# Performance work log

Hardware: AMD Instinct MI355X
Metric: run time of the kernel (lower is better)

Reference implementation:

```python
import jax, jax.numpy as jnp
import numpy as np
from jax import lax
import math

POOL = 7
SPATIAL_SCALE = 0.125
SCORE_THRESH = 0.05
NMS_THRESH = 0.5
DET_PER_IMG = 100
NUM_CLASSES = 81
NUM_STAGES = 3
FEAT_CH = 256
CLIP_VAL = math.log(1000.0 / 16)
STDS = ((0.1, 0.1, 0.2, 0.2), (0.05, 0.05, 0.1, 0.1), (0.033, 0.033, 0.067, 0.067))


def setup_inputs() -> dict:
    key = jax.random.key(0)
    ks = jax.random.split(key, 12)
    B, N, img = 2, 512, 512
    features = jax.random.normal(ks[0], (B, FEAT_CH, 64, 64), jnp.float32)
    cx = jax.random.uniform(ks[1], (B, N)) * img
    cy = jax.random.uniform(ks[2], (B, N)) * img
    w = 16.0 + jax.random.uniform(ks[3], (B, N)) * 240.0
    h = 16.0 + jax.random.uniform(ks[4], (B, N)) * 240.0
    proposals = jnp.stack([
        jnp.clip(cx - 0.5 * w, 0.0, img), jnp.clip(cy - 0.5 * h, 0.0, img),
        jnp.clip(cx + 0.5 * w, 0.0, img), jnp.clip(cy + 0.5 * h, 0.0, img)], axis=-1)
    in_dim = FEAT_CH * POOL * POOL
    sc = 0.02
    return {
        'features': features,
        'proposals': proposals,
        'fc1_w': jax.random.normal(ks[5], (NUM_STAGES, in_dim, 1024), jnp.float32) * sc,
        'fc1_b': jnp.zeros((NUM_STAGES, 1024), jnp.float32),
        'fc2_w': jax.random.normal(ks[6], (NUM_STAGES, 1024, 1024), jnp.float32) * sc,
        'fc2_b': jnp.zeros((NUM_STAGES, 1024), jnp.float32),
        'cls_w': jax.random.normal(ks[7], (NUM_STAGES, 1024, NUM_CLASSES), jnp.float32) * sc,
        'cls_b': jnp.zeros((NUM_STAGES, NUM_CLASSES), jnp.float32),
        'bbox_w': jax.random.normal(ks[8], (NUM_STAGES, 1024, 4), jnp.float32) * sc,
        'bbox_b': jnp.zeros((NUM_STAGES, 4), jnp.float32),
        'image_size': 512,
    }


def _bilinear(feat, gx, gy):
    # feat [C,H,W]; gx,gy [N,P,P] float coords
    C, H, W = feat.shape
    x = jnp.clip(gx, 0.0, W - 1.0)
    y = jnp.clip(gy, 0.0, H - 1.0)
    x0f, y0f = jnp.floor(x), jnp.floor(y)
    x0 = x0f.astype(jnp.int32)
    y0 = y0f.astype(jnp.int32)
    x1 = jnp.minimum(x0 + 1, W - 1)
    y1 = jnp.minimum(y0 + 1, H - 1)
    dx = (x - x0f)[None]
    dy = (y - y0f)[None]
    v = (feat[:, y0, x0] * (1 - dy) * (1 - dx) + feat[:, y0, x1] * (1 - dy) * dx
         + feat[:, y1, x0] * dy * (1 - dx) + feat[:, y1, x1] * dy * dx)
    return v  # [C,N,P,P]


def roi_align(feat, boxes):
    # feat [C,H,W], boxes [N,4] in feature-map coords
    x1, y1, x2, y2 = boxes[:, 0], boxes[:, 1], boxes[:, 2], boxes[:, 3]
    bw = jnp.maximum(x2 - x1, 1.0) / POOL
    bh = jnp.maximum(y2 - y1, 1.0) / POOL
    c = jnp.arange(POOL, dtype=boxes.dtype) + 0.5
    xs = x1[:, None] + c * bw[:, None]  # [N,P]
    ys = y1[:, None] + c * bh[:, None]
    N = boxes.shape[0]
    gx = jnp.broadcast_to(xs[:, None, :], (N, POOL, POOL))
    gy = jnp.broadcast_to(ys[:, :, None], (N, POOL, POOL))
    return jnp.transpose(_bilinear(feat, gx, gy), (1, 0, 2, 3))  # [N,C,P,P]


def decode_boxes(proposals, deltas, stds):
    px1, py1, px2, py2 = proposals[:, 0], proposals[:, 1], proposals[:, 2], proposals[:, 3]
    pw = jnp.maximum(px2 - px1, 1e-6)
    ph = jnp.maximum(py2 - py1, 1e-6)
    pcx = px1 + 0.5 * pw
    pcy = py1 + 0.5 * ph
    wx, wy, ww, wh = stds
    dx = deltas[:, 0] * wx
    dy = deltas[:, 1] * wy
    dw = jnp.minimum(deltas[:, 2] * ww, CLIP_VAL)
    dh = jnp.minimum(deltas[:, 3] * wh, CLIP_VAL)
    cx = dx * pw + pcx
    cy = dy * ph + pcy
    w = jnp.exp(dw) * pw
    h = jnp.exp(dh) * ph
    return jnp.stack([cx - 0.5 * w, cy - 0.5 * h, cx + 0.5 * w, cy + 0.5 * h], axis=1)


def clip_boxes(b, img):
    return jnp.stack([jnp.clip(b[:, 0], 0.0, img), jnp.clip(b[:, 1], 0.0, img),
                      jnp.clip(b[:, 2], 0.0, img), jnp.clip(b[:, 3], 0.0, img)], axis=1)


def nms_per_image(boxes, probs, img):
    # boxes [N,4], probs [N,C]
    N, C = probs.shape
    Cm = C - 1  # skip background class 0
    labels = jnp.broadcast_to(jnp.arange(1, C, dtype=jnp.int32), (N, Cm)).reshape(-1)
    b = jnp.broadcast_to(boxes[:, None, :], (N, Cm, 4)).reshape(-1, 4)
    s = probs[:, 1:].reshape(-1)
    ws = b[:, 2] - b[:, 0]
    hs = b[:, 3] - b[:, 1]
    valid = (s > SCORE_THRESH) & (ws >= 1.0) & (hs >= 1.0)
    s = jnp.where(valid, s, -1.0)
    # class-offset trick == batched_nms
    ob = b + (labels.astype(b.dtype) * (img + 2.0))[:, None]
    area = jnp.maximum(ob[:, 2] - ob[:, 0], 0.0) * jnp.maximum(ob[:, 3] - ob[:, 1], 0.0)

    def step(s_live, _):
        i = jnp.argmax(s_live)
        si = s_live[i]
        bi = ob[i]
        ix1 = jnp.maximum(bi[0], ob[:, 0])
        iy1 = jnp.maximum(bi[1], ob[:, 1])
        ix2 = jnp.minimum(bi[2], ob[:, 2])
        iy2 = jnp.minimum(bi[3], ob[:, 3])
        inter = jnp.maximum(ix2 - ix1, 0.0) * jnp.maximum(iy2 - iy1, 0.0)
        iou = inter / (area[i] + area - inter + 1e-9)
        s_live = jnp.where(iou > NMS_THRESH, -1.0, s_live)
        s_live = s_live.at[i].set(-1.0)
        return s_live, (i, si)

    _, (idx, sel_s) = lax.scan(step, s, None, length=DET_PER_IMG)
    flag = sel_s > 0.0
    out_boxes = jnp.where(flag[:, None], b[idx], 0.0)
    out_scores = jnp.where(flag, sel_s, 0.0)
    out_labels = jnp.where(flag, labels[idx], 0)
    return out_boxes, out_scores, out_labels


def reference(features, proposals, fc1_w, fc1_b, fc2_w, fc2_b, cls_w, cls_b, bbox_w, bbox_b, image_size):
    B, Cf, H, W = features.shape
    N = proposals.shape[1]
    img = float(image_size)
    cur = proposals  # [B,N,4]
    logits = None
    for st in range(NUM_STAGES):
        pooled = jax.vmap(lambda f, bx: roi_align(f, bx * SPATIAL_SCALE))(features, cur)  # [B,N,C,P,P]
        x = pooled.reshape(B * N, -1)
        x = jax.nn.relu(x @ fc1_w[st] + fc1_b[st])
        x = jax.nn.relu(x @ fc2_w[st] + fc2_b[st])
        logits = x @ cls_w[st] + cls_b[st]  # [B*N, C]
        deltas = x @ bbox_w[st] + bbox_b[st]  # [B*N, 4]
        dec = clip_boxes(decode_boxes(cur.reshape(-1, 4), deltas, STDS[st]), img)
        cur = dec.reshape(B, N, 4)
    probs = jax.nn.softmax(logits.reshape(B, N, -1), axis=-1)
    boxes, scores, labels = jax.vmap(lambda bb, pp: nms_per_image(bb, pp, img))(cur, probs)
    return boxes, scores, labels
```

## Files before the change

kernel.cpp:

```cpp
#include <hip/hip_runtime.h>
#include <math.h>

#define NPROP 512
#define NB 2
#define NROWS (NB*NPROP)
#define FCH 256
#define FH 64
#define FW 64
#define INDIM (FCH*7*7)
#define HID 1024
#define NCLS 81
#define CAND_PER_IMG (NPROP*(NCLS-1))
#define CLIPV 4.1351666f

typedef _Float16 f16x8 __attribute__((ext_vector_type(8)));
typedef float f32x4 __attribute__((ext_vector_type(4)));
typedef unsigned int u32;
typedef unsigned long long u64;

__device__ __forceinline__ void gload16(const void* g, void* l) {
    __builtin_amdgcn_global_load_lds((const __attribute__((address_space(1))) u32*)g,
                                     (__attribute__((address_space(3))) u32*)l, 16, 0, 0);
}

#define XHI_OFF    0ull
#define XLO_OFF    25690112ull
#define WT1HI_OFF  51380224ull
#define WT1LO_OFF  77070336ull
#define WT2HI_OFF  102760448ull
#define WT2LO_OFF  104857600ull
#define H1HI_OFF   106954752ull
#define H1LO_OFF   109051904ull
#define H2_OFF     111149056ull
#define CWT_OFF    115343360ull
#define BWT_OFF    116338688ull
#define PROBS_OFF  116387840ull
#define CUR_OFF    116719616ull
#define CNT_OFF    116736000ull
#define CCS_OFF    116737024ull
#define CCOB_OFF   117064704ull
#define CCAR_OFF   118375424ull
#define CCBX_OFF   118703104ull
#define CCIX_OFF   120013824ull
#define SVS_OFF    120341504ull
#define SVB_OFF    120423424ull
#define SVI_OFF    120751104ull
#define SVC_OFF    120833024ull
#define PART_OFF   121489408ull

__global__ void init_kernel(int* ccnt) {
    if (threadIdx.x < 160) ccnt[threadIdx.x] = 0;
}

__global__ __launch_bounds__(256) void roi_align_kernel(
    const float* __restrict__ feat, const float* __restrict__ boxes,
    _Float16* __restrict__ Xhi, _Float16* __restrict__ Xlo)
{
    int r = blockIdx.x;
    int b = r >> 9;
    const float* f = feat + (size_t)b * (FCH*FH*FW);
    __shared__ float sb[4];
    __shared__ int   sx0[49], sx1[49], sy0[49], sy1[49];
    __shared__ float sw00[49], sw01[49], sw10[49], sw11[49];
    int tid = threadIdx.x;
    if (tid == 0) {
        float x1 = boxes[r*4+0]*0.125f, y1 = boxes[r*4+1]*0.125f;
        float x2 = boxes[r*4+2]*0.125f, y2 = boxes[r*4+3]*0.125f;
        sb[0] = x1; sb[1] = y1;
        sb[2] = fmaxf(x2-x1, 1.0f) / 7.0f;
        sb[3] = fmaxf(y2-y1, 1.0f) / 7.0f;
    }
    __syncthreads();
    if (tid < 49) {
        int py = tid / 7, px = tid - py*7;
        float gx = sb[0] + ((float)px + 0.5f)*sb[2];
        float gy = sb[1] + ((float)py + 0.5f)*sb[3];
        gx = fminf(fmaxf(gx, 0.0f), 63.0f);
        gy = fminf(fmaxf(gy, 0.0f), 63.0f);
        float x0f = floorf(gx), y0f = floorf(gy);
        int x0 = (int)x0f, y0 = (int)y0f;
        sx0[tid] = x0; sy0[tid] = y0;
        sx1[tid] = min(x0+1, 63); sy1[tid] = min(y0+1, 63);
        float dx = gx - x0f, dy = gy - y0f;
        sw00[tid] = (1.0f-dy)*(1.0f-dx);
        sw01[tid] = (1.0f-dy)*dx;
        sw10[tid] = dy*(1.0f-dx);
        sw11[tid] = dy*dx;
    }
    __syncthreads();
    size_t xbase = (size_t)r * INDIM;
    for (int i = tid; i < INDIM; i += 256) {
        int c = i / 49;
        int p = i - c*49;
        const float* fc = f + c*(FH*FW);
        int r0 = sy0[p]*FW, r1 = sy1[p]*FW;
        float v = fc[r0 + sx0[p]]*sw00[p] + fc[r0 + sx1[p]]*sw01[p]
                + fc[r1 + sx0[p]]*sw10[p] + fc[r1 + sx1[p]]*sw11[p];
        float vs = v * 32.0f;
        _Float16 h = (_Float16)vs;
        Xhi[xbase + i] = h;
        Xlo[xbase + i] = (_Float16)(vs - (float)h);
    }
}

__global__ __launch_bounds__(256) void trans_limb(
    const float* __restrict__ in, _Float16* __restrict__ hi, _Float16* __restrict__ lo,
    int K, int N, float scale)
{
    __shared__ float t[32][33];
    int tx = threadIdx.x & 31, ty = threadIdx.x >> 5;
    int n0 = blockIdx.x << 5, k0 = blockIdx.y << 5;
#pragma unroll
    for (int r = 0; r < 4; ++r)
        t[ty + 8*r][tx] = in[(size_t)(k0 + ty + 8*r)*N + n0 + tx];
    __syncthreads();
#pragma unroll
    for (int r = 0; r < 4; ++r) {
        int n = n0 + ty + 8*r, k = k0 + tx;
        float v = t[tx][ty + 8*r] * scale;
        _Float16 h = (_Float16)v;
        hi[(size_t)n*K + k] = h;
        lo[(size_t)n*K + k] = (_Float16)(v - (float)h);
    }
}

__global__ __launch_bounds__(256) void trans_naive(
    const float* __restrict__ in, float* __restrict__ out, int K, int N, int batch)
{
    int idx = blockIdx.x*256 + threadIdx.x;
    int per = K*N;
    if (idx >= per*batch) return;
    int b = idx / per;
    int rem = idx - b*per;
    int n = rem / K, k = rem - n*K;
    out[idx] = in[(size_t)b*per + (size_t)k*N + n];
}

__global__ __launch_bounds__(256) void mfma_gemm_limb(
    const _Float16* __restrict__ Ahi, const _Float16* __restrict__ Alo,
    const _Float16* __restrict__ Bhi, const _Float16* __restrict__ Blo,
    float* __restrict__ part, int K, int base, int extra, int lognz)
{
    __shared__ __align__(16) _Float16 lds[2][4][512][8];
    const int tid = threadIdx.x;
    const int lane = tid & 63;
    const int w = tid >> 6, wm = w >> 1, wn = w & 1;
    const int kg = lane >> 4, lr = lane & 15;
    const int bid = blockIdx.x;
    const int nzm = (1 << lognz) - 1;
    const int z = bid & nzm;
    const int bx = (bid >> lognz) & 7;
    const int by = bid >> (lognz + 3);
    const int row0 = by << 7, col0 = bx << 7;
    const int zsteps = base + (z < extra ? 1 : 0);
    const int kb0 = (z*base + (z < extra ? z : extra)) * 32;
    const int r_ = tid & 127;
    const int ks1 = tid >> 7;
    const int wb = tid & 192;

    const _Float16* srcA0 = Ahi + (size_t)(row0 + r_) * K + kb0 + ks1*8;
    const _Float16* srcA1 = Alo + (size_t)(row0 + r_) * K + kb0 + ks1*8;
    const _Float16* srcB0 = Bhi + (size_t)(col0 + r_) * K + kb0 + ks1*8;
    const _Float16* srcB1 = Blo + (size_t)(col0 + r_) * K + kb0 + ks1*8;

    f32x4 acc[4][4];
#pragma unroll
    for (int i = 0; i < 4; ++i)
#pragma unroll
        for (int j = 0; j < 4; ++j) acc[i][j] = (f32x4){0.f, 0.f, 0.f, 0.f};

#define STAGE(bf, off) do { \
    _Float16* Lb = &lds[bf][0][0][0]; \
    gload16(srcA0 + (off),      (void*)(Lb + (0*512 +       wb)*8)); \
    gload16(srcA0 + (off) + 16, (void*)(Lb + (0*512 + 256 + wb)*8)); \
    gload16(srcA1 + (off),      (void*)(Lb + (1*512 +       wb)*8)); \
    gload16(srcA1 + (off) + 16, (void*)(Lb + (1*512 + 256 + wb)*8)); \
    gload16(srcB0 + (off),      (void*)(Lb + (2*512 +       wb)*8)); \
    gload16(srcB0 + (off) + 16, (void*)(Lb + (2*512 + 256 + wb)*8)); \
    gload16(srcB1 + (off),      (void*)(Lb + (3*512 +       wb)*8)); \
    gload16(srcB1 + (off) + 16, (void*)(Lb + (3*512 + 256 + wb)*8)); \
} while (0)

    STAGE(0, 0);
    if (1 < zsteps) STAGE(1, 32);
    for (int t = 0; t < zsteps; ++t) {
        if (t + 1 < zsteps) asm volatile("s_waitcnt vmcnt(8)" ::: "memory");
        else                asm volatile("s_waitcnt vmcnt(0)" ::: "memory");
        __builtin_amdgcn_s_barrier();
        const _Float16* Lr = &lds[t & 1][0][0][0];
        f16x8 Ah[4], Al[4], Bh[4], Bl[4];
#pragma unroll
        for (int mi = 0; mi < 4; ++mi) {
            int s = kg*128 + wm*64 + mi*16 + lr;
            Ah[mi] = *(const f16x8*)(Lr + (0*512 + s)*8);
            Al[mi] = *(const f16x8*)(Lr + (1*512 + s)*8);
        }
#pragma unroll
        for (int ni = 0; ni < 4; ++ni) {
            int s = kg*128 + wn*64 + ni*16 + lr;
            Bh[ni] = *(const f16x8*)(Lr + (2*512 + s)*8);
            Bl[ni] = *(const f16x8*)(Lr + (3*512 + s)*8);
        }
        asm volatile("s_waitcnt lgkmcnt(0)" ::: "memory");
        __builtin_amdgcn_sched_barrier(0);
        __builtin_amdgcn_s_barrier();
        if (t + 2 < zsteps) STAGE(t & 1, (t+2)*32);
#pragma unroll
        for (int mi = 0; mi < 4; ++mi)
#pragma unroll
            for (int ni = 0; ni < 4; ++ni) {
                acc[mi][ni] = __builtin_amdgcn_mfma_f32_16x16x32_f16(Ah[mi], Bh[ni], acc[mi][ni], 0, 0, 0);
                acc[mi][ni] = __builtin_amdgcn_mfma_f32_16x16x32_f16(Ah[mi], Bl[ni], acc[mi][ni], 0, 0, 0);
                acc[mi][ni] = __builtin_amdgcn_mfma_f32_16x16x32_f16(Al[mi], Bh[ni], acc[mi][ni], 0, 0, 0);
            }
    }
#undef STAGE

    float* cb = part + ((size_t)z << 20)
              + (size_t)row0*HID + col0 + wn*64 + lr;
#pragma unroll
    for (int mi = 0; mi < 4; ++mi) {
#pragma unroll
        for (int j = 0; j < 4; ++j) {
            int row = wm*64 + mi*16 + kg*4 + j;
            float* pr = cb + (size_t)row*HID;
            pr[0]  = acc[mi][0][j];
            pr[16] = acc[mi][1][j];
            pr[32] = acc[mi][2][j];
            pr[48] = acc[mi][3][j];
        }
    }
}

__global__ __launch_bounds__(256) void reduce_bias_relu(
    const float* __restrict__ part, const float* __restrict__ bias,
    float* __restrict__ out32, _Float16* __restrict__ outhi, _Float16* __restrict__ outlo,
    int nsplit, int mode)
{
    int gid = blockIdx.x*256 + threadIdx.x;
    float s = 0.f;
    for (int p = 0; p < nsplit; ++p) s += part[((size_t)p << 20) + gid];
    s = s * (1.0f/2048.0f) + bias[gid & (HID-1)];
    s = fmaxf(s, 0.f);
    if (mode == 0) {
        out32[gid] = s;
    } else {
        float vs = s * 32.0f;
        _Float16 h = (_Float16)vs;
        outhi[gid] = h;
        outlo[gid] = (_Float16)(vs - (float)h);
    }
}

__global__ __launch_bounds__(512) void heads_kernel(
    const float* __restrict__ X, const float* __restrict__ cwT, const float* __restrict__ cb,
    const float* __restrict__ bwT, const float* __restrict__ bbb,
    float* __restrict__ cur, float* __restrict__ probs,
    const int* __restrict__ img_sz, int stage, int write_probs)
{
    __shared__ float xs[4][1024];
    __shared__ float lg[4][96];
    int tid = threadIdx.x;
    int lr = tid >> 7;
    int j  = tid & 127;
    int row0 = blockIdx.x * 4;
    for (int i = tid; i < 4096; i += 512)
        xs[i >> 10][i & 1023] = X[(size_t)(row0 + (i >> 10))*1024 + (i & 1023)];
    __syncthreads();
    int row = row0 + lr;
    if (j < 85) {
        const float* wrow = (j < 81) ? (cwT + (size_t)j*HID) : (bwT + (size_t)(j-81)*HID);
        float acc = (j < 81) ? cb[j] : bbb[j-81];
        const float4* w4 = (const float4*)wrow;
#pragma unroll 4
        for (int k4 = 0; k4 < 256; ++k4) {
            float4 wv = w4[k4];
            const float* xr = &xs[lr][k4*4];
            acc = fmaf(xr[0], wv.x, acc);
            acc = fmaf(xr[1], wv.y, acc);
            acc = fmaf(xr[2], wv.z, acc);
            acc = fmaf(xr[3], wv.w, acc);
        }
        lg[lr][j] = acc;
    }
    __syncthreads();
    if (j == 0) {
        float img = (float)(*img_sz);
        float px1 = cur[row*4+0], py1 = cur[row*4+1];
        float px2 = cur[row*4+2], py2 = cur[row*4+3];
        float pw = fmaxf(px2-px1, 1e-6f), ph = fmaxf(py2-py1, 1e-6f);
        float pcx = px1 + 0.5f*pw, pcy = py1 + 0.5f*ph;
        float wx, wy, ww, wh;
        if (stage == 0)      { wx=0.1f;   wy=0.1f;   ww=0.2f;   wh=0.2f;   }
        else if (stage == 1) { wx=0.05f;  wy=0.05f;  ww=0.1f;   wh=0.1f;   }
        else                 { wx=0.033f; wy=0.033f; ww=0.067f; wh=0.067f; }
        float dx = lg[lr][81]*wx, dy = lg[lr][82]*wy;
        float dw = fminf(lg[lr][83]*ww, CLIPV);
        float dh = fminf(lg[lr][84]*wh, CLIPV);
        float cx = dx*pw + pcx, cy = dy*ph + pcy;
        float w = expf(dw)*pw, h = expf(dh)*ph;
        cur[row*4+0] = fminf(fmaxf(cx - 0.5f*w, 0.f), img);
        cur[row*4+1] = fminf(fmaxf(cy - 0.5f*h, 0.f), img);
        cur[row*4+2] = fminf(fmaxf(cx + 0.5f*w, 0.f), img);
        cur[row*4+3] = fminf(fmaxf(cy + 0.5f*h, 0.f), img);
    }
    if (write_probs) {
        if (j == 1) {
            float m = lg[lr][0];
            for (int c2 = 1; c2 < 81; ++c2) m = fmaxf(m, lg[lr][c2]);
            float s = 0.f;
            for (int c2 = 0; c2 < 81; ++c2) s += expf(lg[lr][c2] - m);
            lg[lr][88] = m; lg[lr][89] = s;
        }
        __syncthreads();
        if (j < 81)
            probs[(size_t)row*81 + j] = expf(lg[lr][j] - lg[lr][88]) / lg[lr][89];
    }
}

__global__ __launch_bounds__(256) void compact_class(
    const float* __restrict__ probs, const float* __restrict__ cur,
    const int* __restrict__ img_sz, int* __restrict__ ccnt,
    float* __restrict__ ccs, float4* __restrict__ ccob, float* __restrict__ ccar,
    float4* __restrict__ ccbx, int* __restrict__ ccix)
{
    int gid = blockIdx.x*256 + threadIdx.x;
    if (gid >= NB*CAND_PER_IMG) return;
    int b = gid / CAND_PER_IMG;
    int rem = gid - b*CAND_PER_IMG;
    int n = rem / 80;
    int cm = rem - n*80;
    int label = cm + 1;
    int r = b*NPROP + n;
    float s = probs[(size_t)r*81 + label];
    float b0 = cur[r*4+0], b1 = cur[r*4+1], b2 = cur[r*4+2], b3 = cur[r*4+3];
    if (s > 0.05f && (b2 - b0) >= 1.0f && (b3 - b1) >= 1.0f) {
        int cls = b*80 + cm;
        int pos = atomicAdd(&ccnt[cls], 1);
        int base = cls*512 + pos;
        float img = (float)(*img_sz);
        float t = (float)label * (img + 2.0f);
        float o0 = b0+t, o1 = b1+t, o2 = b2+t, o3 = b3+t;
        ccs[base] = s;
        ccob[base] = make_float4(o0, o1, o2, o3);
        ccar[base] = fmaxf(o2-o0, 0.f) * fmaxf(o3-o1, 0.f);
        ccbx[base] = make_float4(b0, b1, b2, b3);
        ccix[base] = rem;
    }
}

__global__ __launch_bounds__(64) void class_nms(
    const int* __restrict__ ccnt, const float* __restrict__ ccs,
    const float4* __restrict__ ccob, const float* __restrict__ ccar,
    const float4* __restrict__ ccbx, const int* __restrict__ ccix,
    float* __restrict__ svs, float4* __restrict__ svb, int* __restrict__ svi,
    int* __restrict__ svc)
{
    int cls = blockIdx.x;
    int Nc = ccnt[cls];
    int base = cls*512;
    int lane = threadIdx.x;
    __shared__ float sel[5];
    float s[8]; float4 ob[8]; float a[8]; int ix[8];
    int cntl = 0;
    for (int j = lane; j < Nc; j += 64) {
        s[cntl] = ccs[base+j]; ob[cntl] = ccob[base+j];
        a[cntl] = ccar[base+j]; ix[cntl] = ccix[base+j];
        ++cntl;
    }
    int svn = 0;
    int rounds = (Nc < 100) ? Nc : 100;
    for (int it = 0; it < rounds; ++it) {
        float bs = -1.f; int bi = 0x7fffffff;
        for (int q = 0; q < cntl; ++q)
            if (s[q] > bs || (s[q] == bs && ix[q] < bi)) { bs = s[q]; bi = ix[q]; }
        for (int off = 32; off > 0; off >>= 1) {
            float os = __shfl_xor(bs, off);
            int oi = __shfl_xor(bi, off);
            if (os > bs || (os == bs && oi < bi)) { bs = os; bi = oi; }
        }
        if (bs <= 0.f) break;
        for (int q = 0; q < cntl; ++q) {
            if (s[q] == bs && ix[q] == bi) {
                sel[0] = ob[q].x; sel[1] = ob[q].y; sel[2] = ob[q].z; sel[3] = ob[q].w;
                sel[4] = a[q];
                int slot = cls*128 + svn;
                svs[slot] = bs;
                svb[slot] = ccbx[base + lane + q*64];
                svi[slot] = bi;
                s[q] = -1.f;
            }
        }
        __syncthreads();
        float bi0 = sel[0], bi1 = sel[1], bi2 = sel[2], bi3 = sel[3], ai = sel[4];
        for (int q = 0; q < cntl; ++q) {
            if (s[q] > 0.f) {
                float ix1 = fmaxf(bi0, ob[q].x), iy1 = fmaxf(bi1, ob[q].y);
                float ix2 = fminf(bi2, ob[q].z), iy2 = fminf(bi3, ob[q].w);
                float inter = fmaxf(ix2-ix1, 0.f) * fmaxf(iy2-iy1, 0.f);
                float iou = inter / (ai + a[q] - inter + 1e-9f);
                if (iou > 0.5f) s[q] = -1.f;
            }
        }
        ++svn;
        __syncthreads();
    }
    if (lane == 0) svc[cls] = svn;
}

__global__ __launch_bounds__(256) void merge_topk(
    const float* __restrict__ svs, const float4* __restrict__ svb,
    const int* __restrict__ svi, const int* __restrict__ svc,
    float* __restrict__ out)
{
    extern __shared__ char smem[];
    u64* keys = (u64*)smem;
    u32* pay  = (u32*)(smem + 65536);
    __shared__ int off[81];
    __shared__ int n2s;
    int b = blockIdx.x, tid = threadIdx.x;
    if (tid == 0) {
        int run = 0;
        for (int c = 0; c < 80; ++c) { off[c] = run; run += svc[b*80 + c]; }
        off[80] = run;
        int n2 = 256;
        while (n2 < run) n2 <<= 1;
        n2s = n2;
    }
    __syncthreads();
    int Ns = off[80], n2 = n2s;
    for (int c = 0; c < 80; ++c) {
        int n = off[c+1] - off[c];
        int srcb = (b*80 + c)*128;
        for (int k = tid; k < n; k += 256) {
            int src = srcb + k;
            keys[off[c] + k] = ((u64)__float_as_uint(svs[src]) << 32)
                             | (u64)(0xFFFFFFFFu - (u32)svi[src]);
            pay[off[c] + k] = src;
        }
    }
    for (int i = Ns + tid; i < n2; i += 256) { keys[i] = 0; pay[i] = 0; }
    __syncthreads();
    for (int k = 2; k <= n2; k <<= 1) {
        for (int j = k >> 1; j > 0; j >>= 1) {
            for (int i = tid; i < n2; i += 256) {
                int l = i ^ j;
                if (l > i) {
                    u64 a = keys[i], bb = keys[l];
                    bool dir = ((i & k) == 0);
                    if ((a < bb) == dir) {
                        keys[i] = bb; keys[l] = a;
                        u32 p = pay[i]; pay[i] = pay[l]; pay[l] = p;
                    }
                }
            }
            __syncthreads();
        }
    }
    if (tid < 100) {
        u64 kk = keys[tid];
        if (kk != 0) {
            u32 ci = 0xFFFFFFFFu - (u32)(kk & 0xFFFFFFFFull);
            float4 bx = svb[pay[tid]];
            out[b*400 + tid*4 + 0] = bx.x;
            out[b*400 + tid*4 + 1] = bx.y;
            out[b*400 + tid*4 + 2] = bx.z;
            out[b*400 + tid*4 + 3] = bx.w;
            out[800  + b*100 + tid] = __uint_as_float((u32)(kk >> 32));
            out[1000 + b*100 + tid] = (float)((ci % 80) + 1);
        } else {
            out[b*400 + tid*4 + 0] = 0.f; out[b*400 + tid*4 + 1] = 0.f;
            out[b*400 + tid*4 + 2] = 0.f; out[b*400 + tid*4 + 3] = 0.f;
            out[800  + b*100 + tid] = 0.f;
            out[1000 + b*100 + tid] = 0.f;
        }
    }
}

extern "C" void kernel_launch(void* const* d_in, const int* in_sizes, int n_in,
                              void* d_out, int out_size, void* d_ws, size_t ws_size,
                              hipStream_t stream)
{
    const float* features  = (const float*)d_in[0];
    const float* proposals = (const float*)d_in[1];
    const float* fc1_w = (const float*)d_in[2];
    const float* fc1_b = (const float*)d_in[3];
    const float* fc2_w = (const float*)d_in[4];
    const float* fc2_b = (const float*)d_in[5];
    const float* cls_w = (const float*)d_in[6];
    const float* cls_b = (const float*)d_in[7];
    const float* bbox_w = (const float*)d_in[8];
    const float* bbox_b = (const float*)d_in[9];
    const int* img_sz = (const int*)d_in[10];
    float* out = (float*)d_out;
    char* ws = (char*)d_ws;
    _Float16* xhi   = (_Float16*)(ws + XHI_OFF);
    _Float16* xlo   = (_Float16*)(ws + XLO_OFF);
    _Float16* wt1hi = (_Float16*)(ws + WT1HI_OFF);
    _Float16* wt1lo = (_Float16*)(ws + WT1LO_OFF);
    _Float16* wt2hi = (_Float16*)(ws + WT2HI_OFF);
    _Float16* wt2lo = (_Float16*)(ws + WT2LO_OFF);
    _Float16* h1hi  = (_Float16*)(ws + H1HI_OFF);
    _Float16* h1lo  = (_Float16*)(ws + H1LO_OFF);
    float*  h2     = (float*) (ws + H2_OFF);
    float*  cwT    = (float*) (ws + CWT_OFF);
    float*  bwT    = (float*) (ws + BWT_OFF);
    float*  probs  = (float*) (ws + PROBS_OFF);
    float*  cur    = (float*) (ws + CUR_OFF);
    int*    ccnt   = (int*)   (ws + CNT_OFF);
    float*  ccs    = (float*) (ws + CCS_OFF);
    float4* ccob   = (float4*)(ws + CCOB_OFF);
    float*  ccar   = (float*) (ws + CCAR_OFF);
    float4* ccbx   = (float4*)(ws + CCBX_OFF);
    int*    ccix   = (int*)   (ws + CCIX_OFF);
    float*  svs    = (float*) (ws + SVS_OFF);
    float4* svb    = (float4*)(ws + SVB_OFF);
    int*    svi    = (int*)   (ws + SVI_OFF);
    int*    svc    = (int*)   (ws + SVC_OFF);
    float*  part   = (float*) (ws + PART_OFF);

    init_kernel<<<1, 256, 0, stream>>>(ccnt);
    hipMemcpyAsync(cur, proposals, (size_t)NROWS*4*sizeof(float),
                   hipMemcpyDeviceToDevice, stream);
    trans_naive<<<(3*NCLS*HID + 255)/256, 256, 0, stream>>>(cls_w, cwT, HID, NCLS, 3);
    trans_naive<<<(3*4*HID + 255)/256, 256, 0, stream>>>(bbox_w, bwT, HID, 4, 3);

    for (int st = 0; st < 3; ++st) {
        roi_align_kernel<<<NROWS, 256, 0, stream>>>(features, cur, xhi, xlo);
        trans_limb<<<dim3(HID/32, INDIM/32), 256, 0, stream>>>(
            fc1_w + (size_t)st*INDIM*HID, wt1hi, wt1lo, INDIM, HID, 64.0f);
        mfma_gemm_limb<<<512, 256, 0, stream>>>(
            xhi, xlo, wt1hi, wt1lo, part, INDIM, 49, 0, 3);
        reduce_bias_relu<<<(NROWS*HID)/256, 256, 0, stream>>>(
            part, fc1_b + st*HID, nullptr, h1hi, h1lo, 8, 1);
        trans_limb<<<dim3(HID/32, HID/32), 256, 0, stream>>>(
            fc2_w + (size_t)st*HID*HID, wt2hi, wt2lo, HID, HID, 64.0f);
        mfma_gemm_limb<<<512, 256, 0, stream>>>(
            h1hi, h1lo, wt2hi, wt2lo, part, HID, 4, 0, 3);
        reduce_bias_relu<<<(NROWS*HID)/256, 256, 0, stream>>>(
            part, fc2_b + st*HID, h2, nullptr, nullptr, 8, 0);
        heads_kernel<<<NROWS/4, 512, 0, stream>>>(
            h2, cwT + (size_t)st*NCLS*HID, cls_b + st*NCLS,
            bwT + (size_t)st*4*HID, bbox_b + st*4,
            cur, probs, img_sz, st, st == 2 ? 1 : 0);
    }
    compact_class<<<(NB*CAND_PER_IMG)/256, 256, 0, stream>>>(
        probs, cur, img_sz, ccnt, ccs, ccob, ccar, ccbx, ccix);
    class_nms<<<160, 64, 0, stream>>>(
        ccnt, ccs, ccob, ccar, ccbx, ccix, svs, svb, svi, svc);
    merge_topk<<<NB, 256, 98304, stream>>>(
        svs, svb, svi, svc, out);
}
```

Measured before the change: 810.7 us.

## Load GEMM fragments directly from global memory into registers, dropping LDS staging

Replaces the LDS double-buffered global_load_lds staging in the limb MFMA GEMM with direct per-wave global loads of f16x8 fragments into registers, software-pipelined with two register fragment sets. This removes the LDS round trip and the block barriers. In exchange each wave loads its own A/B fragments, so data is no longer shared through LDS between the waves that read the same rows or columns, and global and L2 traffic rise. Launch bounds are set to one block per SM to allow more registers.

```diff
diff --git a/kernel.cpp b/kernel.cpp
--- a/kernel.cpp
+++ b/kernel.cpp
@@ -17,11 +17,6 @@
 typedef float f32x4 __attribute__((ext_vector_type(4)));
 typedef unsigned int u32;
 typedef unsigned long long u64;
-
-__device__ __forceinline__ void gload16(const void* g, void* l) {
-    __builtin_amdgcn_global_load_lds((const __attribute__((address_space(1))) u32*)g,
-                                     (__attribute__((address_space(3))) u32*)l, 16, 0, 0);
-}
 
 #define XHI_OFF    0ull
 #define XLO_OFF    25690112ull
@@ -136,12 +131,37 @@
     out[idx] = in[(size_t)b*per + (size_t)k*N + n];
 }
 
-__global__ __launch_bounds__(256) void mfma_gemm_limb(
+struct Frags { f16x8 Ah[4], Al[4], Bh[4], Bl[4]; };
+
+__device__ __forceinline__ void loadf(
+    Frags& F, const _Float16* pAh, const _Float16* pAl,
+    const _Float16* pBh, const _Float16* pBl, size_t KS, int koff)
+{
+#pragma unroll
+    for (int i = 0; i < 4; ++i) {
+        F.Ah[i] = *(const f16x8*)(pAh + i*KS + koff);
+        F.Al[i] = *(const f16x8*)(pAl + i*KS + koff);
+        F.Bh[i] = *(const f16x8*)(pBh + i*KS + koff);
+        F.Bl[i] = *(const f16x8*)(pBl + i*KS + koff);
+    }
+}
+
+__device__ __forceinline__ void mfma16(Frags& F, f32x4 (&acc)[4][4]) {
+#pragma unroll
+    for (int mi = 0; mi < 4; ++mi)
+#pragma unroll
+        for (int ni = 0; ni < 4; ++ni) {
+            acc[mi][ni] = __builtin_amdgcn_mfma_f32_16x16x32_f16(F.Ah[mi], F.Bh[ni], acc[mi][ni], 0, 0, 0);
+            acc[mi][ni] = __builtin_amdgcn_mfma_f32_16x16x32_f16(F.Ah[mi], F.Bl[ni], acc[mi][ni], 0, 0, 0);
+            acc[mi][ni] = __builtin_amdgcn_mfma_f32_16x16x32_f16(F.Al[mi], F.Bh[ni], acc[mi][ni], 0, 0, 0);
+        }
+}
+
+__global__ __launch_bounds__(256, 1) void mfma_gemm_limb(
     const _Float16* __restrict__ Ahi, const _Float16* __restrict__ Alo,
     const _Float16* __restrict__ Bhi, const _Float16* __restrict__ Blo,
     float* __restrict__ part, int K, int base, int extra, int lognz)
 {
-    __shared__ __align__(16) _Float16 lds[2][4][512][8];
     const int tid = threadIdx.x;
     const int lane = tid & 63;
     const int w = tid >> 6, wm = w >> 1, wn = w & 1;
@@ -154,14 +174,14 @@
     const int row0 = by << 7, col0 = bx << 7;
     const int zsteps = base + (z < extra ? 1 : 0);
     const int kb0 = (z*base + (z < extra ? z : extra)) * 32;
-    const int r_ = tid & 127;
-    const int ks1 = tid >> 7;
-    const int wb = tid & 192;
-
-    const _Float16* srcA0 = Ahi + (size_t)(row0 + r_) * K + kb0 + ks1*8;
-    const _Float16* srcA1 = Alo + (size_t)(row0 + r_) * K + kb0 + ks1*8;
-    const _Float16* srcB0 = Bhi + (size_t)(col0 + r_) * K + kb0 + ks1*8;
-    const _Float16* srcB1 = Blo + (size_t)(col0 + r_) * K + kb0 + ks1*8;
+
+    const size_t aoff = (size_t)(row0 + wm*64 + lr) * K + kb0 + kg*8;
+    const size_t boff = (size_t)(col0 + wn*64 + lr) * K + kb0 + kg*8;
+    const _Float16* pAh = Ahi + aoff;
+    const _Float16* pAl = Alo + aoff;
+    const _Float16* pBh = Bhi + boff;
+    const _Float16* pBl = Blo + boff;
+    const size_t KS = (size_t)K * 16;
 
     f32x4 acc[4][4];
 #pragma unroll
@@ -169,52 +189,18 @@
 #pragma unroll
         for (int j = 0; j < 4; ++j) acc[i][j] = (f32x4){0.f, 0.f, 0.f, 0.f};
 
-#define STAGE(bf, off) do { \
-    _Float16* Lb = &lds[bf][0][0][0]; \
-    gload16(srcA0 + (off),      (void*)(Lb + (0*512 +       wb)*8)); \
-    gload16(srcA0 + (off) + 16, (void*)(Lb + (0*512 + 256 + wb)*8)); \
-    gload16(srcA1 + (off),      (void*)(Lb + (1*512 +       wb)*8)); \
-    gload16(srcA1 + (off) + 16, (void*)(Lb + (1*512 + 256 + wb)*8)); \
-    gload16(srcB0 + (off),      (void*)(Lb + (2*512 +       wb)*8)); \
-    gload16(srcB0 + (off) + 16, (void*)(Lb + (2*512 + 256 + wb)*8)); \
-    gload16(srcB1 + (off),      (void*)(Lb + (3*512 +       wb)*8)); \
-    gload16(srcB1 + (off) + 16, (void*)(Lb + (3*512 + 256 + wb)*8)); \
-} while (0)
-
-    STAGE(0, 0);
-    if (1 < zsteps) STAGE(1, 32);
-    for (int t = 0; t < zsteps; ++t) {
-        if (t + 1 < zsteps) asm volatile("s_waitcnt vmcnt(8)" ::: "memory");
-        else                asm volatile("s_waitcnt vmcnt(0)" ::: "memory");
-        __builtin_amdgcn_s_barrier();
-        const _Float16* Lr = &lds[t & 1][0][0][0];
-        f16x8 Ah[4], Al[4], Bh[4], Bl[4];
-#pragma unroll
-        for (int mi = 0; mi < 4; ++mi) {
-            int s = kg*128 + wm*64 + mi*16 + lr;
-            Ah[mi] = *(const f16x8*)(Lr + (0*512 + s)*8);
-            Al[mi] = *(const f16x8*)(Lr + (1*512 + s)*8);
-        }
-#pragma unroll
-        for (int ni = 0; ni < 4; ++ni) {
-            int s = kg*128 + wn*64 + ni*16 + lr;
-            Bh[ni] = *(const f16x8*)(Lr + (2*512 + s)*8);
-            Bl[ni] = *(const f16x8*)(Lr + (3*512 + s)*8);
-        }
-        asm volatile("s_waitcnt lgkmcnt(0)" ::: "memory");
-        __builtin_amdgcn_sched_barrier(0);
-        __builtin_amdgcn_s_barrier();
-        if (t + 2 < zsteps) STAGE(t & 1, (t+2)*32);
-#pragma unroll
-        for (int mi = 0; mi < 4; ++mi)
-#pragma unroll
-            for (int ni = 0; ni < 4; ++ni) {
-                acc[mi][ni] = __builtin_amdgcn_mfma_f32_16x16x32_f16(Ah[mi], Bh[ni], acc[mi][ni], 0, 0, 0);
-                acc[mi][ni] = __builtin_amdgcn_mfma_f32_16x16x32_f16(Ah[mi], Bl[ni], acc[mi][ni], 0, 0, 0);
-                acc[mi][ni] = __builtin_amdgcn_mfma_f32_16x16x32_f16(Al[mi], Bh[ni], acc[mi][ni], 0, 0, 0);
-            }
-    }
-#undef STAGE
+    Frags F0, F1;
+    loadf(F0, pAh, pAl, pBh, pBl, KS, 0);
+    int t = 0;
+    while (t < zsteps) {
+        if (t + 1 < zsteps) loadf(F1, pAh, pAl, pBh, pBl, KS, (t+1)*32);
+        mfma16(F0, acc);
+        ++t;
+        if (t >= zsteps) break;
+        if (t + 1 < zsteps) loadf(F0, pAh, pAl, pBh, pBl, KS, (t+1)*32);
+        mfma16(F1, acc);
+        ++t;
+    }
 
     float* cb = part + ((size_t)z << 20)
               + (size_t)row0*HID + col0 + wn*64 + lr;
```

Result: slower. 1.058 ms (+30.4%).

## Use 256x256-tile split-K MFMA GEMM with 512 threads for fc1

Applied to the files above, without the earlier changes.

Adds a new fc1 GEMM kernel that uses 256x256 output tiles, 8 waves per block and a 128KB double-buffered LDS staged through global_load_lds. It uses 16-way split-K in place of the previous 128x128 tiles with 8-way split-K. The larger tile is meant to raise arithmetic intensity and cut repeated global loads of the hi/lo fp16 limbs. In exchange there is heavy register pressure from 32 accumulators per wave, lower occupancy, and twice as many partial buffers for the reduction to read.

```diff
diff --git a/kernel.cpp b/kernel.cpp
--- a/kernel.cpp
+++ b/kernel.cpp
@@ -134,6 +134,98 @@
     int rem = idx - b*per;
     int n = rem / K, k = rem - n*K;
     out[idx] = in[(size_t)b*per + (size_t)k*N + n];
+}
+
+__global__ __launch_bounds__(512, 2) void mfma_gemm_limb256(
+    const _Float16* __restrict__ Ahi, const _Float16* __restrict__ Alo,
+    const _Float16* __restrict__ Bhi, const _Float16* __restrict__ Blo,
+    float* __restrict__ part, int K, int base, int extra)
+{
+    extern __shared__ __align__(16) char ldsraw[];
+    const int tid = threadIdx.x;
+    const int lane = tid & 63;
+    const int w = tid >> 6;
+    const int wm = w >> 2, wn = w & 3;
+    const int kg = lane >> 4, lr = lane & 15;
+    const int bid = blockIdx.x;
+    const int z = bid & 15;
+    const int tile = bid >> 4;
+    const int bx = tile & 3, by = tile >> 2;
+    const int row0 = by << 8, col0 = bx << 8;
+    const int zsteps = base + (z < extra ? 1 : 0);
+    const int kb0 = (z*base + (z < extra ? z : extra)) * 32;
+
+    const int sp = w >> 1;
+    const int sbase = (w & 1) * 8;
+    const _Float16* pl = (sp == 0) ? Ahi : (sp == 1) ? Alo : (sp == 2) ? Bhi : Blo;
+    const int rc0 = (sp < 2) ? row0 : col0;
+    const _Float16* sG = pl + (size_t)(rc0 + lane)*K + kb0;
+
+    f32x4 acc[8][4];
+#pragma unroll
+    for (int i = 0; i < 8; ++i)
+#pragma unroll
+        for (int j = 0; j < 4; ++j) acc[i][j] = (f32x4){0.f, 0.f, 0.f, 0.f};
+
+    auto STAGE = [&](int bufoff, int koff) {
+#pragma unroll
+        for (int j = 0; j < 8; ++j) {
+            int sub = sbase + j;
+            int ks = sub >> 2, rblk = sub & 3;
+            const void* g = (const void*)(sG + (size_t)(rblk*64)*K + koff + ks*8);
+            void* l = (void*)(ldsraw + bufoff + sp*16384 + ks*4096 + rblk*1024);
+            gload16(g, l);
+        }
+    };
+
+    STAGE(0, 0);
+    if (zsteps > 1) STAGE(65536, 32);
+
+    for (int t = 0; t < zsteps; ++t) {
+        if (t + 1 < zsteps) asm volatile("s_waitcnt vmcnt(8)" ::: "memory");
+        else                asm volatile("s_waitcnt vmcnt(0)" ::: "memory");
+        __builtin_amdgcn_s_barrier();
+        asm volatile("" ::: "memory");
+        const char* Lb = ldsraw + ((t & 1) ? 65536 : 0);
+        f16x8 Bh[4], Bl[4];
+#pragma unroll
+        for (int ni = 0; ni < 4; ++ni) {
+            int s = (kg*256 + wn*64 + ni*16 + lr) * 16;
+            Bh[ni] = *(const f16x8*)(Lb + 2*16384 + s);
+            Bl[ni] = *(const f16x8*)(Lb + 3*16384 + s);
+        }
+#pragma unroll
+        for (int mi = 0; mi < 8; ++mi) {
+            int s = (kg*256 + wm*128 + mi*16 + lr) * 16;
+            f16x8 ah = *(const f16x8*)(Lb + s);
+            f16x8 al = *(const f16x8*)(Lb + 16384 + s);
+#pragma unroll
+            for (int ni = 0; ni < 4; ++ni) {
+                acc[mi][ni] = __builtin_amdgcn_mfma_f32_16x16x32_f16(ah, Bh[ni], acc[mi][ni], 0, 0, 0);
+                acc[mi][ni] = __builtin_amdgcn_mfma_f32_16x16x32_f16(ah, Bl[ni], acc[mi][ni], 0, 0, 0);
+                acc[mi][ni] = __builtin_amdgcn_mfma_f32_16x16x32_f16(al, Bh[ni], acc[mi][ni], 0, 0, 0);
+            }
+        }
+        asm volatile("" ::: "memory");
+        __builtin_amdgcn_s_barrier();
+        asm volatile("" ::: "memory");
+        if (t + 2 < zsteps) STAGE((t & 1) ? 65536 : 0, (t+2)*32);
+    }
+
+    float* cb = part + ((size_t)z << 20)
+              + (size_t)row0*HID + col0 + wn*64 + lr;
+#pragma unroll
+    for (int mi = 0; mi < 8; ++mi) {
+#pragma unroll
+        for (int j = 0; j < 4; ++j) {
+            int row = wm*128 + mi*16 + kg*4 + j;
+            float* pr = cb + (size_t)row*HID;
+            pr[0]  = acc[mi][0][j];
+            pr[16] = acc[mi][1][j];
+            pr[32] = acc[mi][2][j];
+            pr[48] = acc[mi][3][j];
+        }
+    }
 }
 
 __global__ __launch_bounds__(256) void mfma_gemm_limb(
@@ -529,10 +621,10 @@
         roi_align_kernel<<<NROWS, 256, 0, stream>>>(features, cur, xhi, xlo);
         trans_limb<<<dim3(HID/32, INDIM/32), 256, 0, stream>>>(
             fc1_w + (size_t)st*INDIM*HID, wt1hi, wt1lo, INDIM, HID, 64.0f);
-        mfma_gemm_limb<<<512, 256, 0, stream>>>(
-            xhi, xlo, wt1hi, wt1lo, part, INDIM, 49, 0, 3);
+        mfma_gemm_limb256<<<256, 512, 131072, stream>>>(
+            xhi, xlo, wt1hi, wt1lo, part, INDIM, 24, 8);
         reduce_bias_relu<<<(NROWS*HID)/256, 256, 0, stream>>>(
-            part, fc1_b + st*HID, nullptr, h1hi, h1lo, 8, 1);
+            part, fc1_b + st*HID, nullptr, h1hi, h1lo, 16, 1);
         trans_limb<<<dim3(HID/32, HID/32), 256, 0, stream>>>(
             fc2_w + (size_t)st*HID*HID, wt2hi, wt2lo, HID, HID, 64.0f);
         mfma_gemm_limb<<<512, 256, 0, stream>>>(
```

Result: faster. 775.3 us (-4.4%).
